# Performance work log

Measured on AMD Instinct MI355X. Metric: run time of the kernel, lower is better.

Reference implementation:

```python
import jax, jax.numpy as jnp
import numpy as np

CHANNELS = 256
NUM_HEADS = 4
GROUPS = 8
EPS = 1e-5


def setup_inputs() -> dict:
    key = jax.random.key(0)
    ks = jax.random.split(key, 5)
    C = CHANNELS
    x = jax.random.normal(ks[0], (2, C, 16, 16, 16), dtype=jnp.float32)
    # GroupNorm affine params
    norm_w = jnp.ones((C,), dtype=jnp.float32)
    norm_b = jnp.zeros((C,), dtype=jnp.float32)
    # 1x1x1 Conv3d weights collapsed to dense matrices [out, in]
    fan = 1.0 / np.sqrt(C)
    qkv_w = jax.random.uniform(ks[1], (3 * C, C), jnp.float32, -fan, fan)
    qkv_b = jax.random.uniform(ks[2], (3 * C,), jnp.float32, -fan, fan)
    proj_w = jax.random.uniform(ks[3], (C, C), jnp.float32, -fan, fan)
    proj_b = jax.random.uniform(ks[4], (C,), jnp.float32, -fan, fan)
    return {"x": x, "norm_w": norm_w, "norm_b": norm_b,
            "qkv_w": qkv_w, "qkv_b": qkv_b,
            "proj_w": proj_w, "proj_b": proj_b}


def _group_norm(x, w, b):
    B, C, D, H, W = x.shape
    xg = x.reshape(B, GROUPS, C // GROUPS, D, H, W)
    mean = xg.mean(axis=(2, 3, 4, 5), keepdims=True)
    var = xg.var(axis=(2, 3, 4, 5), keepdims=True)
    xn = (xg - mean) * jax.lax.rsqrt(var + EPS)
    xn = xn.reshape(B, C, D, H, W)
    return xn * w[None, :, None, None, None] + b[None, :, None, None, None]


def reference(x, norm_w, norm_b, qkv_w, qkv_b, proj_w, proj_b):
    B, C, D, H, W = x.shape
    N = D * H * W
    hd = C // NUM_HEADS
    h = _group_norm(x, norm_w, norm_b)
    # 1x1x1 conv == channel matmul: [B, 3C, N]
    hf = h.reshape(B, C, N)
    qkv = jnp.einsum('oc,bcn->bon', qkv_w, hf) + qkv_b[None, :, None]
    q, k, v = jnp.split(qkv, 3, axis=1)
    q = q.reshape(B, NUM_HEADS, hd, N)
    k = k.reshape(B, NUM_HEADS, hd, N)
    v = v.reshape(B, NUM_HEADS, hd, N)
    scale = hd ** (-0.5)
    attn = jax.nn.softmax(jnp.einsum('bhcn,bhcm->bhnm', q, k) * scale, axis=-1)
    o = jnp.einsum('bhnm,bhcm->bhcn', attn, v)  # [B, H, hd, N]
    o = o.reshape(B, C, N)
    o = jnp.einsum('oc,bcn->bon', proj_w, o) + proj_b[None, :, None]
    return x + o.reshape(B, C, D, H, W)
```

## Files before the change

kernel.cpp:

```cpp
#include <hip/hip_runtime.h>
#include <hip/hip_bf16.h>

#define BATCH 2
#define CH 256
#define NH 4
#define HD 64
#define NGROUP 8
#define CPG 32
#define NTOK 4096
#define EPSV 1e-5f
#define QSCALE 0.1803368801111204f
#define NSPLIT 4

typedef __attribute__((ext_vector_type(8))) short short8;
typedef __attribute__((ext_vector_type(4))) short s4bf;
typedef __attribute__((ext_vector_type(4))) float float4v;

__device__ __forceinline__ unsigned short f2bf(float f) {
    union { float f; unsigned u; } v; v.f = f;
    unsigned r = v.u + 0x7FFF + ((v.u >> 16) & 1);
    return (unsigned short)(r >> 16);
}
__device__ __forceinline__ unsigned short f2bf_fast(float f) {
    union { float f; unsigned u; } v; v.f = f;
    return (unsigned short)((v.u + 0x8000u) >> 16);
}
__device__ __forceinline__ float bf2f(unsigned short u) {
    union { unsigned u; float f; } v; v.u = ((unsigned)u) << 16;
    return v.f;
}
__device__ __forceinline__ unsigned pk2bf(float a, float b) {
#if __has_builtin(__builtin_amdgcn_cvt_pk_bf16_f32)
    typedef __attribute__((ext_vector_type(2))) __bf16 bf2v;
    bf2v p = __builtin_amdgcn_cvt_pk_bf16_f32(a, b);
    union { bf2v v; unsigned u; } c; c.v = p;
    return c.u;
#else
    return (unsigned)f2bf_fast(a) | ((unsigned)f2bf_fast(b) << 16);
#endif
}

#define GL2LDS(g, l) __builtin_amdgcn_global_load_lds( \
    (const __attribute__((address_space(1))) void*)(g), \
    (__attribute__((address_space(3))) void*)(l), 16, 0, 0)

__global__ void prep(const float* __restrict__ x,
                     const float* __restrict__ qkv_w, const float* __restrict__ qkv_b,
                     const float* __restrict__ proj_w,
                     float* __restrict__ psum, float* __restrict__ psq,
                     unsigned short* __restrict__ wq, float* __restrict__ bq,
                     unsigned short* __restrict__ wp) {
    int bx = blockIdx.x;
    int t = threadIdx.x;
    if (bx < 256) {
        int s = bx & 15, g = (bx >> 4) & 7, b = bx >> 7;
        const float* base = x + ((size_t)(b * CH + g * CPG)) * NTOK + (size_t)s * 8192;
        float sum = 0.f, sq = 0.f;
        const float4v* p4 = (const float4v*)base;
        for (int i = 0; i < 8; ++i) {
            float4v v = p4[t + i * 256];
            for (int j = 0; j < 4; ++j) { sum += v[j]; sq += v[j] * v[j]; }
        }
        for (int off = 32; off; off >>= 1) {
            sum += __shfl_down(sum, off, 64);
            sq  += __shfl_down(sq,  off, 64);
        }
        __shared__ float ls[8];
        int wave = t >> 6, lane = t & 63;
        if (lane == 0) { ls[wave * 2] = sum; ls[wave * 2 + 1] = sq; }
        __syncthreads();
        if (t == 0) {
            float S = 0.f, Q = 0.f;
            for (int w = 0; w < 4; ++w) { S += ls[w * 2]; Q += ls[w * 2 + 1]; }
            int idx = (b * NGROUP + g) * 16 + s;
            psum[idx] = S; psq[idx] = Q;
        }
    } else {
        int idx = (bx - 256) * 256 + t;
        int stride = 256 * 256;
        for (int i = idx; i < 3 * CH * CH; i += stride) {
            float f = qkv_w[i];
            if (i < CH * CH) f *= QSCALE;
            wq[i] = f2bf(f);
        }
        for (int i = idx; i < CH * CH; i += stride) wp[i] = f2bf(proj_w[i]);
        for (int i = idx; i < 3 * CH; i += stride) {
            float f = qkv_b[i];
            if (i < CH) f *= QSCALE;
            bq[i] = f;
        }
    }
}

__global__ __launch_bounds__(256) void qkv_gemm(const float* __restrict__ x,
        const float* __restrict__ nw, const float* __restrict__ nb_,
        const float* __restrict__ psum, const float* __restrict__ psq,
        const unsigned short* __restrict__ wq, const float* __restrict__ bq,
        unsigned short* __restrict__ qT, unsigned short* __restrict__ kT,
        unsigned short* __restrict__ vv) {
    int f = blockIdx.x + 64 * blockIdx.y + 768 * blockIdx.z;
    int xcd = f & 7, j = f >> 3;
    int ob = j % 12;
    int p  = xcd + 8 * (j / 12);
    int nb = p & 63;
    int b  = p >> 6;
    int t = threadIdx.x;
    int wave = t >> 6, lane = t & 63;
    int l15 = lane & 15, quad = lane >> 4;
    int o0 = ob * 64 + wave * 16;

    __shared__ __align__(16) unsigned short bt[64 * 264];
    __shared__ float wch[256], bch[256];

    {
        int c = t;
        int gg = c >> 5;
        float S = 0.f, Q = 0.f;
        for (int s = 0; s < 16; ++s) {
            S += psum[(b * NGROUP + gg) * 16 + s];
            Q += psq[(b * NGROUP + gg) * 16 + s];
        }
        const float M = (float)(CPG * NTOK);
        float mean = S / M;
        float inv  = rsqrtf(Q / M - mean * mean + EPSV);
        float w = nw[c] * inv;
        wch[c] = w;
        bch[c] = nb_[c] - mean * w;
    }

    short8 aW[8];
    {
        const unsigned short* wr = wq + (size_t)(o0 + l15) * CH + quad * 8;
        for (int kc = 0; kc < 8; ++kc) aW[kc] = *(const short8*)(wr + kc * 32);
    }
    __syncthreads();

    {
        int n = t & 63, jj = t >> 6;
        const float* xb = x + (size_t)b * CH * NTOK + (size_t)nb * 64 + n;
        for (int i = 0; i < 16; ++i) {
            int c0 = i * 16 + jj * 4;
            float h0 = xb[(size_t)(c0 + 0) * NTOK] * wch[c0 + 0] + bch[c0 + 0];
            float h1 = xb[(size_t)(c0 + 1) * NTOK] * wch[c0 + 1] + bch[c0 + 1];
            float h2 = xb[(size_t)(c0 + 2) * NTOK] * wch[c0 + 2] + bch[c0 + 2];
            float h3 = xb[(size_t)(c0 + 3) * NTOK] * wch[c0 + 3] + bch[c0 + 3];
            union { s4bf v; unsigned u[2]; } pk;
            pk.u[0] = pk2bf(h0, h1);
            pk.u[1] = pk2bf(h2, h3);
            *(s4bf*)(bt + n * 264 + c0) = pk.v;
        }
    }
    __syncthreads();

    float4v acc[4];
    for (int nt = 0; nt < 4; ++nt) for (int r = 0; r < 4; ++r) acc[nt][r] = 0.f;
    for (int kc = 0; kc < 8; ++kc) {
        for (int nt = 0; nt < 4; ++nt) {
            short8 pb = *(const short8*)(bt + (nt * 16 + l15) * 264 + kc * 32 + quad * 8);
            acc[nt] = __builtin_amdgcn_mfma_f32_16x16x32_bf16(aW[kc], pb, acc[nt], 0, 0, 0);
        }
    }
    int seg = ob >> 2;
    if (seg < 2) {
        int hh = ob & 3;
        unsigned short* dst = (seg == 0) ? qT : kT;
        unsigned short* ot = bt;
        __syncthreads();
        for (int nt = 0; nt < 4; ++nt) {
            int ob_ = o0 + quad * 4;
            s4bf pk;
            for (int r = 0; r < 4; ++r)
                pk[r] = (short)f2bf(acc[nt][r] + bq[ob_ + r]);
            int ci = wave * 16 + quad * 4;
            *(s4bf*)(ot + (nt * 16 + l15) * 72 + ci) = pk;
        }
        __syncthreads();
        for (int ii = 0; ii < 2; ++ii) {
            int id2 = ii * 256 + t;
            int n = id2 >> 3, c16 = id2 & 7;
            short8 row = *(const short8*)(ot + n * 72 + c16 * 8);
            *(short8*)(dst + (((size_t)b * NH + hh) * NTOK + (size_t)nb * 64 + n) * HD + c16 * 8) = row;
        }
    } else {
        int hh = ob & 3;
        unsigned short* ot = bt;
        __syncthreads();
        for (int nt = 0; nt < 4; ++nt) {
            int cib = wave * 16 + quad * 4;
            int ob_ = o0 + quad * 4;
            for (int r = 0; r < 4; ++r)
                ot[(cib + r) * 72 + nt * 16 + l15] = f2bf(acc[nt][r] + bq[ob_ + r]);
        }
        __syncthreads();
        for (int ii = 0; ii < 2; ++ii) {
            int id2 = ii * 256 + t;
            int ci = id2 >> 3, c16 = id2 & 7;
            short8 row = *(const short8*)(ot + ci * 72 + c16 * 8);
            *(short8*)(vv + (((size_t)b * NH + hh) * HD + ci) * NTOK + (size_t)nb * 64 + c16 * 8) = row;
        }
    }
}

__global__ __launch_bounds__(256, 4) void attn_kernel(const unsigned short* __restrict__ qT,
        const unsigned short* __restrict__ kT, const unsigned short* __restrict__ vv,
        unsigned short* __restrict__ opb, float* __restrict__ lpb) {
    int f = blockIdx.x + 32 * blockIdx.y + 128 * blockIdx.z;
    int xcd = f & 7, j = f >> 3;
    int nb = j >> 2;
    int g  = xcd + 8 * (j & 3);
    int h  = g & 3;
    int zb = g >> 2;
    int sp = zb & 3, b = zb >> 2;
    int t = threadIdx.x, wave = t >> 6, lane = t & 63;
    int l15 = lane & 15, quad = lane >> 4;
    int n0 = nb * 128 + wave * 32;
    int kv0 = sp * (NTOK / NSPLIT);

    unsigned short* opart = opb + (size_t)sp * ((size_t)BATCH * NTOK * CH);
    float* lpart = lpb + (size_t)sp * (BATCH * NH * NTOK);

    const unsigned short* qbh = qT + ((size_t)(b * NH + h)) * NTOK * HD;
    const unsigned short* kbh = kT + ((size_t)(b * NH + h)) * NTOK * HD;
    const unsigned short* vbh = vv + ((size_t)(b * NH + h)) * HD * NTOK;

    __shared__ __align__(16) unsigned short kbuf[2][64 * 64];
    __shared__ __align__(16) unsigned short vbuf[2][64 * 64];

    short8 aQ[2][2];
    for (int mt = 0; mt < 2; ++mt) {
        aQ[mt][0] = *(const short8*)(qbh + (size_t)(n0 + mt * 16 + l15) * HD + quad * 8);
        aQ[mt][1] = *(const short8*)(qbh + (size_t)(n0 + mt * 16 + l15) * HD + 32 + quad * 8);
    }

    float l_p[2] = {0.f, 0.f};
    float4v o_acc[2][4];
    for (int mt = 0; mt < 2; ++mt)
        for (int ct = 0; ct < 4; ++ct)
            for (int r = 0; r < 4; ++r) o_acc[mt][ct][r] = 0.f;
    const float4v ZERO = {0.f, 0.f, 0.f, 0.f};

    int sl0 = (wave * 2 + 0) * 64 + lane, sl1 = (wave * 2 + 1) * 64 + lane;
    int r0 = sl0 >> 3, c0 = sl0 & 7, r1 = sl1 >> 3, c1 = sl1 & 7;
    const unsigned short* kga0 = kbh + (size_t)(kv0 + r0) * HD + ((c0 ^ (r0 & 7)) << 3);
    const unsigned short* kga1 = kbh + (size_t)(kv0 + r1) * HD + ((c1 ^ (r1 & 7)) << 3);
    const unsigned short* vga0 = vbh + (size_t)r0 * NTOK + kv0 + ((c0 ^ (r0 & 7)) << 3);
    const unsigned short* vga1 = vbh + (size_t)r1 * NTOK + kv0 + ((c1 ^ (r1 & 7)) << 3);

    #define STAGE_ADV(kb_, vb_)                                   \
        do {                                                      \
            GL2LDS(kga0, (kb_) + (wave * 2 + 0) * 512);           \
            GL2LDS(kga1, (kb_) + (wave * 2 + 1) * 512);           \
            GL2LDS(vga0, (vb_) + (wave * 2 + 0) * 512);           \
            GL2LDS(vga1, (vb_) + (wave * 2 + 1) * 512);           \
            kga0 += 64 * HD; kga1 += 64 * HD;                     \
            vga0 += 64;      vga1 += 64;                          \
        } while (0)

    STAGE_ADV(kbuf[0], vbuf[0]);
    int cur = 0;

    for (int ms = kv0; ms < kv0 + NTOK / NSPLIT; ms += 64) {
        asm volatile("s_waitcnt vmcnt(0)" ::: "memory");
        __syncthreads();
        if (ms + 64 < kv0 + NTOK / NSPLIT)
            STAGE_ADV(kbuf[cur ^ 1], vbuf[cur ^ 1]);
        const unsigned short* kb = kbuf[cur];
        const unsigned short* vb = vbuf[cur];

        float4v s[2][4];
        __builtin_amdgcn_s_setprio(1);
#pragma unroll
        for (int nt = 0; nt < 4; ++nt) {
            int krow = nt * 16 + l15;
            int r7 = krow & 7;
            short8 ak0 = *(const short8*)(kb + krow * 64 + ((quad ^ r7) << 3));
            short8 ak1 = *(const short8*)(kb + krow * 64 + (((quad + 4) ^ r7) << 3));
#pragma unroll
            for (int mt = 0; mt < 2; ++mt) {
                float4v z = __builtin_amdgcn_mfma_f32_16x16x32_bf16(ak0, aQ[mt][0], ZERO, 0, 0, 0);
                z = __builtin_amdgcn_mfma_f32_16x16x32_bf16(ak1, aQ[mt][1], z, 0, 0, 0);
                s[mt][nt] = z;
            }
        }
        __builtin_amdgcn_s_setprio(0);
        s4bf aP[2][4];
#pragma unroll
        for (int mt = 0; mt < 2; ++mt) {
#pragma unroll
            for (int nt = 0; nt < 4; ++nt) {
                float e0 = __builtin_amdgcn_exp2f(s[mt][nt][0]);
                float e1 = __builtin_amdgcn_exp2f(s[mt][nt][1]);
                float e2 = __builtin_amdgcn_exp2f(s[mt][nt][2]);
                float e3 = __builtin_amdgcn_exp2f(s[mt][nt][3]);
                l_p[mt] += (e0 + e1) + (e2 + e3);
                union { s4bf v; unsigned u[2]; } c;
                c.u[0] = pk2bf(e0, e1);
                c.u[1] = pk2bf(e2, e3);
                aP[mt][nt] = c.v;
            }
        }
        __builtin_amdgcn_s_setprio(1);
#pragma unroll
        for (int ct = 0; ct < 4; ++ct) {
#pragma unroll
            for (int nt = 0; nt < 4; ++nt) {
                int vr = ct * 16 + l15;
                int c8 = nt * 2 + (quad >> 1);
                s4bf bv = *(const s4bf*)(vb + vr * 64 +
                                         ((c8 ^ (vr & 7)) << 3) + ((quad & 1) << 2));
#pragma unroll
                for (int mt = 0; mt < 2; ++mt)
                    o_acc[mt][ct] = __builtin_amdgcn_mfma_f32_16x16x16bf16_1k(aP[mt][nt], bv, o_acc[mt][ct], 0, 0, 0);
            }
        }
        __builtin_amdgcn_s_setprio(0);
        cur ^= 1;
    }
    for (int mt = 0; mt < 2; ++mt) {
        l_p[mt] += __shfl_xor(l_p[mt], 16, 64);
        l_p[mt] += __shfl_xor(l_p[mt], 32, 64);
    }
    for (int mt = 0; mt < 2; ++mt) {
        for (int ct = 0; ct < 4; ++ct) {
            for (int r = 0; r < 4; ++r) {
                int n = n0 + mt * 16 + quad * 4 + r;
                int cg = h * HD + ct * 16 + l15;
                opart[((size_t)b * NTOK + n) * CH + cg] = f2bf(o_acc[mt][ct][r]);
            }
        }
        if (lane < 16)
            lpart[((size_t)(b * NH + h)) * NTOK + n0 + mt * 16 + lane] = l_p[mt];
    }
}

__global__ __launch_bounds__(256) void proj_gemm(const unsigned short* __restrict__ opb,
        const float* __restrict__ lpb, const unsigned short* __restrict__ wp,
        const float* __restrict__ proj_b, const float* __restrict__ x,
        float* __restrict__ out) {
    int f = blockIdx.x + 64 * blockIdx.y + 256 * blockIdx.z;
    int xcd = f & 7, j = f >> 3;
    int cb = j & 3;
    int p  = xcd + 8 * (j >> 2);
    int nb = p & 63;
    int b  = p >> 6;
    int t = threadIdx.x, wave = t >> 6, lane = t & 63;
    int l15 = lane & 15, quad = lane >> 4;
    int c0 = cb * 64 + wave * 16;
    const size_t OP = (size_t)BATCH * NTOK * CH;
    const size_t LP = (size_t)BATCH * NH * NTOK;

    __shared__ __align__(16) unsigned short bt[64 * 264];
    __shared__ float rl[64 * 4];

    short8 aW[8];
    {
        const unsigned short* wr = wp + (size_t)(c0 + l15) * CH + quad * 8;
        for (int kc = 0; kc < 8; ++kc) aW[kc] = *(const short8*)(wr + kc * 32);
    }
    {
        int r = t >> 2, h = t & 3;
        size_t lidx = ((size_t)(b * NH + h)) * NTOK + nb * 64 + r;
        float ls = (lpb[lidx] + lpb[LP + lidx]) + (lpb[2 * LP + lidx] + lpb[3 * LP + lidx]);
        rl[r * 4 + h] = 1.0f / ls;
    }
    __syncthreads();
    for (int p2 = 0; p2 < 8; ++p2) {
        int slot = p2 * 256 + t;
        int r = slot >> 5, c = slot & 31;
        size_t base = ((size_t)b * NTOK + nb * 64 + r) * CH + c * 8;
        short8 o0 = *(const short8*)(opb + base);
        short8 o1 = *(const short8*)(opb + OP + base);
        short8 o2 = *(const short8*)(opb + 2 * OP + base);
        short8 o3 = *(const short8*)(opb + 3 * OP + base);
        float rinv = rl[r * 4 + (c >> 3)];
        short8 m;
        for (int jj = 0; jj < 8; ++jj) {
            float ff = (bf2f((unsigned short)o0[jj]) + bf2f((unsigned short)o1[jj]))
                     + (bf2f((unsigned short)o2[jj]) + bf2f((unsigned short)o3[jj]));
            m[jj] = (short)f2bf(ff * rinv);
        }
        *(short8*)(bt + r * 264 + c * 8) = m;
    }
    __syncthreads();

    float4v acc[4];
    for (int nt = 0; nt < 4; ++nt) for (int r = 0; r < 4; ++r) acc[nt][r] = 0.f;
    for (int kc = 0; kc < 8; ++kc) {
        for (int nt = 0; nt < 4; ++nt) {
            short8 pb = *(const short8*)(bt + (nt * 16 + l15) * 264 + kc * 32 + quad * 8);
            acc[nt] = __builtin_amdgcn_mfma_f32_16x16x32_bf16(aW[kc], pb, acc[nt], 0, 0, 0);
        }
    }
    for (int nt = 0; nt < 4; ++nt) {
        int n = nb * 64 + nt * 16 + l15;
        for (int r = 0; r < 4; ++r) {
            int cc = c0 + quad * 4 + r;
            size_t idx = ((size_t)(b * CH + cc)) * NTOK + n;
            out[idx] = acc[nt][r] + proj_b[cc] + x[idx];
        }
    }
}

extern "C" void kernel_launch(void* const* d_in, const int* in_sizes, int n_in,
                              void* d_out, int out_size, void* d_ws, size_t ws_size,
                              hipStream_t stream) {
    const float* x      = (const float*)d_in[0];
    const float* norm_w = (const float*)d_in[1];
    const float* norm_b = (const float*)d_in[2];
    const float* qkv_w  = (const float*)d_in[3];
    const float* qkv_b  = (const float*)d_in[4];
    const float* proj_w = (const float*)d_in[5];
    const float* proj_b = (const float*)d_in[6];
    float* out = (float*)d_out;

    char* ws = (char*)d_ws;
    float* psum  = (float*)ws;
    float* psq   = (float*)(ws + 1024);
    float* bqs   = (float*)(ws + 4096);
    unsigned short* wqb = (unsigned short*)(ws + 8192);
    unsigned short* wpb = (unsigned short*)(ws + 401408);
    float* lpb = (float*)(ws + 532480);
    const size_t MB4 = 4194304;
    unsigned short* opb = (unsigned short*)(ws + 2097152);
    unsigned short* qT = (unsigned short*)(ws + 2097152 + 4 * MB4);
    unsigned short* kT = (unsigned short*)(ws + 2097152 + 5 * MB4);
    unsigned short* vv = (unsigned short*)(ws + 2097152 + 6 * MB4);

    prep<<<dim3(512), dim3(256), 0, stream>>>(x, qkv_w, qkv_b, proj_w, psum, psq, wqb, bqs, wpb);
    qkv_gemm<<<dim3(64, 12, BATCH), dim3(256), 0, stream>>>(x, norm_w, norm_b, psum, psq,
                                                            wqb, bqs, qT, kT, vv);
    attn_kernel<<<dim3(32, NH, BATCH * NSPLIT), dim3(256), 0, stream>>>(qT, kT, vv, opb, lpb);
    proj_gemm<<<dim3(64, 4, BATCH), dim3(256), 0, stream>>>(opb, lpb, wpb, proj_b, x, out);
}
```

Baseline: 146.0 us.

## Drop LDS double-buffering in attention; read K/V fragments directly from global

Removes the shared-memory staging of K and V tiles (async global-to-LDS loads, double buffer, per-iteration barrier and vmcnt wait). Each wave now loads its MFMA operand fragments straight from global memory, relying on L1/L2 for reuse across the four waves of a block. This removes barrier and LDS overhead but multiplies global/cache traffic by the number of waves and exposes load latency without explicit prefetch.

Result: slower. 270.8 us (+85.5%).

```diff
diff --git a/kernel.cpp b/kernel.cpp
--- a/kernel.cpp
+++ b/kernel.cpp
@@ -39,10 +39,6 @@
     return (unsigned)f2bf_fast(a) | ((unsigned)f2bf_fast(b) << 16);
 #endif
 }
-
-#define GL2LDS(g, l) __builtin_amdgcn_global_load_lds( \
-    (const __attribute__((address_space(1))) void*)(g), \
-    (__attribute__((address_space(3))) void*)(l), 16, 0, 0)
 
 __global__ void prep(const float* __restrict__ x,
                      const float* __restrict__ qkv_w, const float* __restrict__ qkv_b,
@@ -223,9 +219,6 @@
     const unsigned short* kbh = kT + ((size_t)(b * NH + h)) * NTOK * HD;
     const unsigned short* vbh = vv + ((size_t)(b * NH + h)) * HD * NTOK;
 
-    __shared__ __align__(16) unsigned short kbuf[2][64 * 64];
-    __shared__ __align__(16) unsigned short vbuf[2][64 * 64];
-
     short8 aQ[2][2];
     for (int mt = 0; mt < 2; ++mt) {
         aQ[mt][0] = *(const short8*)(qbh + (size_t)(n0 + mt * 16 + l15) * HD + quad * 8);
@@ -239,42 +232,17 @@
             for (int r = 0; r < 4; ++r) o_acc[mt][ct][r] = 0.f;
     const float4v ZERO = {0.f, 0.f, 0.f, 0.f};
 
-    int sl0 = (wave * 2 + 0) * 64 + lane, sl1 = (wave * 2 + 1) * 64 + lane;
-    int r0 = sl0 >> 3, c0 = sl0 & 7, r1 = sl1 >> 3, c1 = sl1 & 7;
-    const unsigned short* kga0 = kbh + (size_t)(kv0 + r0) * HD + ((c0 ^ (r0 & 7)) << 3);
-    const unsigned short* kga1 = kbh + (size_t)(kv0 + r1) * HD + ((c1 ^ (r1 & 7)) << 3);
-    const unsigned short* vga0 = vbh + (size_t)r0 * NTOK + kv0 + ((c0 ^ (r0 & 7)) << 3);
-    const unsigned short* vga1 = vbh + (size_t)r1 * NTOK + kv0 + ((c1 ^ (r1 & 7)) << 3);
-
-    #define STAGE_ADV(kb_, vb_)                                   \
-        do {                                                      \
-            GL2LDS(kga0, (kb_) + (wave * 2 + 0) * 512);           \
-            GL2LDS(kga1, (kb_) + (wave * 2 + 1) * 512);           \
-            GL2LDS(vga0, (vb_) + (wave * 2 + 0) * 512);           \
-            GL2LDS(vga1, (vb_) + (wave * 2 + 1) * 512);           \
-            kga0 += 64 * HD; kga1 += 64 * HD;                     \
-            vga0 += 64;      vga1 += 64;                          \
-        } while (0)
-
-    STAGE_ADV(kbuf[0], vbuf[0]);
-    int cur = 0;
+    const unsigned short* krow_base = kbh + (size_t)l15 * HD + quad * 8;
+    const unsigned short* vrow_base = vbh + (size_t)l15 * NTOK + quad * 4;
 
     for (int ms = kv0; ms < kv0 + NTOK / NSPLIT; ms += 64) {
-        asm volatile("s_waitcnt vmcnt(0)" ::: "memory");
-        __syncthreads();
-        if (ms + 64 < kv0 + NTOK / NSPLIT)
-            STAGE_ADV(kbuf[cur ^ 1], vbuf[cur ^ 1]);
-        const unsigned short* kb = kbuf[cur];
-        const unsigned short* vb = vbuf[cur];
-
         float4v s[2][4];
         __builtin_amdgcn_s_setprio(1);
 #pragma unroll
         for (int nt = 0; nt < 4; ++nt) {
-            int krow = nt * 16 + l15;
-            int r7 = krow & 7;
-            short8 ak0 = *(const short8*)(kb + krow * 64 + ((quad ^ r7) << 3));
-            short8 ak1 = *(const short8*)(kb + krow * 64 + (((quad + 4) ^ r7) << 3));
+            const unsigned short* kr = krow_base + (size_t)(ms + nt * 16) * HD;
+            short8 ak0 = *(const short8*)(kr);
+            short8 ak1 = *(const short8*)(kr + 32);
 #pragma unroll
             for (int mt = 0; mt < 2; ++mt) {
                 float4v z = __builtin_amdgcn_mfma_f32_16x16x32_bf16(ak0, aQ[mt][0], ZERO, 0, 0, 0);
@@ -301,20 +269,16 @@
         }
         __builtin_amdgcn_s_setprio(1);
 #pragma unroll
-        for (int ct = 0; ct < 4; ++ct) {
-#pragma unroll
-            for (int nt = 0; nt < 4; ++nt) {
-                int vr = ct * 16 + l15;
-                int c8 = nt * 2 + (quad >> 1);
-                s4bf bv = *(const s4bf*)(vb + vr * 64 +
-                                         ((c8 ^ (vr & 7)) << 3) + ((quad & 1) << 2));
+        for (int nt = 0; nt < 4; ++nt) {
+#pragma unroll
+            for (int ct = 0; ct < 4; ++ct) {
+                s4bf bv = *(const s4bf*)(vrow_base + (size_t)(ct * 16) * NTOK + ms + nt * 16);
 #pragma unroll
                 for (int mt = 0; mt < 2; ++mt)
                     o_acc[mt][ct] = __builtin_amdgcn_mfma_f32_16x16x16bf16_1k(aP[mt][nt], bv, o_acc[mt][ct], 0, 0, 0);
             }
         }
         __builtin_amdgcn_s_setprio(0);
-        cur ^= 1;
     }
     for (int mt = 0; mt < 2; ++mt) {
         l_p[mt] += __shfl_xor(l_p[mt], 16, 64);
```
